# Performance work log

Measured on AMD Instinct MI355X. Metric: run time of the kernel, lower is better.

Reference implementation:

```python
import jax, jax.numpy as jnp
import numpy as np

D_MODEL = 1024
N_HEADS = 16
HEAD_DIM = D_MODEL // N_HEADS
CHUNK = 128
B, T = 2, 2048


def setup_inputs() -> dict:
    key = jax.random.key(0)
    ks = jax.random.split(key, 5)
    x = jax.random.normal(ks[0], (B, T, D_MODEL), dtype=jnp.float32)
    mk = lambda k: jax.random.normal(k, (D_MODEL, D_MODEL), dtype=jnp.float32) * 0.02
    return {"x": x, "Wq": mk(ks[1]), "Wk": mk(ks[2]), "Wv": mk(ks[3]), "Wo": mk(ks[4])}


def _chunked_causal_attention(q, k, v, cs):
    # q,k,v: [B,H,T,D] fp32. Streaming online-softmax over kv chunks (flash-attn style).
    Bq, H, Tq, D = q.shape
    n = Tq // cs  # T divisible by chunk_size
    inv_sqrt_d = 1.0 / (D ** 0.5)
    qc = jnp.moveaxis(q.reshape(Bq, H, n, cs, D), 2, 0)  # [n,B,H,cs,D]
    kc = jnp.moveaxis(k.reshape(Bq, H, n, cs, D), 2, 0)
    vc = jnp.moveaxis(v.reshape(Bq, H, n, cs, D), 2, 0)
    ar = jnp.arange(cs)

    def per_q(qi, qb):  # qb: [B,H,cs,D]
        q_idx = qi * cs + ar

        def step(carry, kv):
            m, l, o = carry
            ki, kb, vb = kv
            s = jnp.einsum('bhqd,bhkd->bhqk', qb, kb) * inv_sqrt_d
            k_idx = ki * cs + ar
            causal = q_idx[:, None] >= k_idx[None, :]
            s = jnp.where(causal, s, -jnp.inf)
            s_max = jnp.max(s, axis=-1, keepdims=True)
            m_new = jnp.maximum(m, s_max)
            # guard fully-masked chunks (m_new = -inf)
            m_safe = jnp.where(jnp.isneginf(m_new), 0.0, m_new)
            alpha = jnp.exp(m - m_safe)
            p = jnp.exp(s - m_safe)
            o = o * alpha + jnp.einsum('bhqk,bhkd->bhqd', p, vb)
            l = l * alpha + jnp.sum(p, axis=-1, keepdims=True)
            return (m_new, l, o), None

        init = (jnp.full((Bq, H, cs, 1), -jnp.inf, dtype=jnp.float32),
                jnp.zeros((Bq, H, cs, 1), dtype=jnp.float32),
                jnp.zeros_like(qb))
        (m, l, o), _ = jax.lax.scan(step, init, (jnp.arange(n), kc, vc))
        return o / jnp.maximum(l, 1e-9)

    out = jax.vmap(per_q)(jnp.arange(n), qc)  # [n,B,H,cs,D]
    return jnp.moveaxis(out, 0, 2).reshape(Bq, H, Tq, D)


def reference(x, Wq, Wk, Wv, Wo):
    Bx, Tx, C = x.shape
    def heads(w):
        return (x @ w.T).reshape(Bx, Tx, N_HEADS, HEAD_DIM).transpose(0, 2, 1, 3)
    q, k, v = heads(Wq), heads(Wk), heads(Wv)
    y = _chunked_causal_attention(q, k, v, CHUNK)  # [B,H,T,D]
    y = y.transpose(0, 2, 1, 3).reshape(Bx, Tx, C)
    return y @ Wo.T
```

## Files before the change

kernel.cpp:

```cpp
#include <hip/hip_runtime.h>
#include <hip/hip_bf16.h>
#include <stdint.h>

typedef __bf16 bf16;
typedef __bf16 bf16x8 __attribute__((ext_vector_type(8)));
typedef __bf16 bf16x4 __attribute__((ext_vector_type(4)));
typedef float  f32x4  __attribute__((ext_vector_type(4)));

#define DM 1024
#define NH 16
#define HD 64
#define TT 2048

#define QSCALE 0.18033688011112042f

__global__ void cvt_all(const float* __restrict__ x,  const float* __restrict__ wq,
                        const float* __restrict__ wk, const float* __restrict__ wv,
                        const float* __restrict__ wo,
                        bf16* __restrict__ xb,  bf16* __restrict__ wqb,
                        bf16* __restrict__ wkb, bf16* __restrict__ wvb,
                        bf16* __restrict__ wob) {
  const int i = (blockIdx.x * blockDim.x + threadIdx.x) * 4;
  const float* src; bf16* dst; int off;
  if (i < 4194304)      { src = x;  dst = xb;  off = i; }
  else {
    const int j = i - 4194304;
    const int w = j >> 20;
    off = j & 1048575;
    src = (w == 0) ? wq : (w == 1) ? wk : (w == 2) ? wv : wo;
    dst = (w == 0) ? wqb : (w == 1) ? wkb : (w == 2) ? wvb : wob;
  }
  const float4 v = *reinterpret_cast<const float4*>(src + off);
  bf16x4 o = { (bf16)v.x, (bf16)v.y, (bf16)v.z, (bf16)v.w };
  *reinterpret_cast<bf16x4*>(dst + off) = o;
}

static __device__ __forceinline__ void gload_lds16(const bf16* g, bf16* l) {
  __builtin_amdgcn_global_load_lds(
      (__attribute__((address_space(1))) void*)g,
      (__attribute__((address_space(3))) void*)l, 16, 0, 0);
}

static __device__ __forceinline__ int swzb(int lin) {
  return lin ^ (((lin >> 7) & 7) << 4);
}

__launch_bounds__(256, 3)
__global__ void gemm_qkv(const bf16* __restrict__ X, const bf16* __restrict__ Wq,
                         const bf16* __restrict__ Wk, const bf16* __restrict__ Wv,
                         bf16* __restrict__ Qb, bf16* __restrict__ Kb,
                         bf16* __restrict__ Vtb) {
  __shared__ bf16 As[128 * 32];
  __shared__ bf16 Bs[128 * 32];
  const int tid  = threadIdx.x;
  const int lane = tid & 63;
  const int wv   = tid >> 6;
  const int lg   = lane >> 4, lc = lane & 15;
  const int m0   = blockIdx.x * 128;
  const int ng   = blockIdx.y * 128;
  const int which = ng >> 10;
  const bf16* W = (which == 0) ? Wq : ((which == 1) ? Wk : Wv);
  const int n0 = ng & 1023;
  const int wm = wv >> 1, wn = wv & 1;

  f32x4 acc[4][4] = {};

  for (int k0 = 0; k0 < DM; k0 += 32) {
#pragma unroll
    for (int c = 0; c < 2; ++c) {
      const int e   = wv * 512 + c * 2048 + lane * 8;
      const int row = e >> 5, col = e & 31;
      gload_lds16(X + (size_t)(m0 + row) * DM + k0 + col, &As[wv * 512 + c * 2048]);
      gload_lds16(W + (size_t)(n0 + row) * DM + k0 + col, &Bs[wv * 512 + c * 2048]);
    }
    __syncthreads();
    bf16x8 a[4], b[4];
#pragma unroll
    for (int i = 0; i < 4; ++i)
      a[i] = *reinterpret_cast<const bf16x8*>(&As[(wm * 64 + i * 16 + lc) * 32 + lg * 8]);
#pragma unroll
    for (int j = 0; j < 4; ++j)
      b[j] = *reinterpret_cast<const bf16x8*>(&Bs[(wn * 64 + j * 16 + lc) * 32 + lg * 8]);
#pragma unroll
    for (int i = 0; i < 4; ++i)
#pragma unroll
      for (int j = 0; j < 4; ++j)
        acc[i][j] = __builtin_amdgcn_mfma_f32_16x16x32_bf16(a[i], b[j], acc[i][j], 0, 0, 0);
    __syncthreads();
  }

#pragma unroll
  for (int i = 0; i < 4; ++i) {
    const int mg = m0 + wm * 64 + i * 16 + lg * 4;
    const int bb = mg >> 11, t = mg & 2047;
#pragma unroll
    for (int j = 0; j < 4; ++j) {
      const int nl = n0 + wn * 64 + j * 16 + lc;
      const int h = nl >> 6, d = nl & 63;
      const int bh = bb * NH + h;
      const f32x4 v = acc[i][j];
      if (which == 0) {
        bf16* p = Qb + ((size_t)bh * TT + t) * HD + d;
#pragma unroll
        for (int r = 0; r < 4; ++r) p[r * HD] = (bf16)(v[r] * QSCALE);
      } else if (which == 1) {
        bf16* p = Kb + ((size_t)bh * TT + t) * HD + d;
#pragma unroll
        for (int r = 0; r < 4; ++r) p[r * HD] = (bf16)v[r];
      } else {
        bf16x4 pk = { (bf16)v[0], (bf16)v[1], (bf16)v[2], (bf16)v[3] };
        *reinterpret_cast<bf16x4*>(Vtb + ((size_t)bh * HD + d) * TT + t) = pk;
      }
    }
  }
}

#define KPAD 72

__launch_bounds__(256, 3)
__global__ void attn_fwd(const bf16* __restrict__ Qb, const bf16* __restrict__ Kb,
                         const bf16* __restrict__ Vtb, bf16* __restrict__ Yb) {
  __shared__ bf16 Ks[2][4096];
  __shared__ bf16 Vs[2][4096];
  __shared__ bf16 Ps[4][16 * KPAD];

  const int tid  = threadIdx.x;
  const int lane = tid & 63;
  const int wv   = tid >> 6;
  const int lg   = lane >> 4;
  const int lc   = lane & 15;
  const int bh   = blockIdx.x & 31;
  const int qblk = 31 - (blockIdx.x >> 5);
  const int q0   = qblk * 64;
  const int NT   = qblk + 1;

  const bf16* Qg = Qb  + (size_t)bh * TT * HD;
  const bf16* Kg = Kb  + (size_t)bh * TT * HD;
  const bf16* Vg = Vtb + (size_t)bh * HD * TT;

  const bf16x8 qf0 = *reinterpret_cast<const bf16x8*>(
      Qg + (size_t)(q0 + wv * 16 + lc) * HD + 0  + lg * 8);
  const bf16x8 qf1 = *reinterpret_cast<const bf16x8*>(
      Qg + (size_t)(q0 + wv * 16 + lc) * HD + 32 + lg * 8);

  int dstb[2], koff[2], voff[2];
#pragma unroll
  for (int c = 0; c < 2; ++c) {
    const int base = (wv * 2 + c) * 1024;
    const int lin  = base + lane * 16;
    dstb[c] = base;
    koff[c] = swzb(lin);
    voff[c] = (lin >> 7) * (TT * 2) + (swzb(lin) & 127);
  }

  auto STAGE = [&](int b, int kv) {
#pragma unroll
    for (int c = 0; c < 2; ++c) {
      gload_lds16((const bf16*)((const char*)Kg + (size_t)kv * 8192 + koff[c]),
                  (bf16*)((char*)Ks[b] + dstb[c]));
      gload_lds16((const bf16*)((const char*)Vg + (size_t)kv * 128 + voff[c]),
                  (bf16*)((char*)Vs[b] + dstb[c]));
    }
  };

  f32x4 o[4] = {};
  float m_run = -INFINITY, l_run = 0.f;
  bf16* Pw = Ps[wv];
  const int b_ = bh >> 4, h_ = bh & 15;
  const int qw = q0 + wv * 16;

  STAGE(0, 0);

  int cur = 0;
  for (int ti = 0; ti < NT; ++ti) {
    const int k0 = ti * 64;

    if (ti + 1 < NT) {
      STAGE(cur ^ 1, ti + 1);
      asm volatile("s_waitcnt vmcnt(4)" ::: "memory");
    } else {
      asm volatile("s_waitcnt vmcnt(0)" ::: "memory");
    }
    __builtin_amdgcn_s_barrier();
    __builtin_amdgcn_sched_barrier(0);

    const char* ksb = (const char*)Ks[cur];
    const char* vsb = (const char*)Vs[cur];

    f32x4 s[4] = {};
    __builtin_amdgcn_s_setprio(1);
#pragma unroll
    for (int kvf = 0; kvf < 4; ++kvf) {
      const bf16x8 k0f = *reinterpret_cast<const bf16x8*>(
          ksb + swzb((kvf * 16 + lc) * 128 + lg * 16));
      s[kvf] = __builtin_amdgcn_mfma_f32_16x16x32_bf16(k0f, qf0, s[kvf], 0, 0, 0);
      const bf16x8 k1f = *reinterpret_cast<const bf16x8*>(
          ksb + swzb((kvf * 16 + lc) * 128 + 64 + lg * 16));
      s[kvf] = __builtin_amdgcn_mfma_f32_16x16x32_bf16(k1f, qf1, s[kvf], 0, 0, 0);
    }
    __builtin_amdgcn_s_setprio(0);

    if (k0 + 63 > qw) {
      const int q = qw + lc;
#pragma unroll
      for (int kvf = 0; kvf < 4; ++kvf)
#pragma unroll
        for (int r = 0; r < 4; ++r)
          if (k0 + kvf * 16 + lg * 4 + r > q) s[kvf][r] = -INFINITY;
    }

    float t0 = fmaxf(fmaxf(s[0][0], s[0][1]), fmaxf(s[0][2], s[0][3]));
    float t1 = fmaxf(fmaxf(s[1][0], s[1][1]), fmaxf(s[1][2], s[1][3]));
    float t2 = fmaxf(fmaxf(s[2][0], s[2][1]), fmaxf(s[2][2], s[2][3]));
    float t3 = fmaxf(fmaxf(s[3][0], s[3][1]), fmaxf(s[3][2], s[3][3]));
    float rmax = fmaxf(fmaxf(t0, t1), fmaxf(t2, t3));
    rmax = fmaxf(rmax, __shfl_xor(rmax, 16));
    rmax = fmaxf(rmax, __shfl_xor(rmax, 32));

    const float mn = fmaxf(m_run, rmax);
    const float alpha = __builtin_amdgcn_exp2f(m_run - mn);
    m_run = mn;

#pragma unroll
    for (int kvf = 0; kvf < 4; ++kvf)
#pragma unroll
      for (int r = 0; r < 4; ++r)
        s[kvf][r] = __builtin_amdgcn_exp2f(s[kvf][r] - mn);

#pragma unroll
    for (int df = 0; df < 4; ++df)
#pragma unroll
      for (int r = 0; r < 4; ++r) o[df][r] *= alpha;

#pragma unroll
    for (int kvf = 0; kvf < 4; ++kvf) {
      bf16x4 pk = { (bf16)s[kvf][0], (bf16)s[kvf][1],
                    (bf16)s[kvf][2], (bf16)s[kvf][3] };
      *reinterpret_cast<bf16x4*>(&Pw[lc * KPAD + kvf * 16 + lg * 4]) = pk;
    }

    __builtin_amdgcn_s_setprio(1);
#pragma unroll
    for (int ks = 0; ks < 2; ++ks) {
      const bf16x8 pf = *reinterpret_cast<const bf16x8*>(
          &Pw[lc * KPAD + ks * 32 + lg * 8]);
#pragma unroll
      for (int df = 0; df < 4; ++df) {
        const bf16x8 vf = *reinterpret_cast<const bf16x8*>(
            vsb + swzb((df * 16 + lc) * 128 + ks * 64 + lg * 16));
        o[df] = __builtin_amdgcn_mfma_f32_16x16x32_bf16(vf, pf, o[df], 0, 0, 0);
      }
    }
    __builtin_amdgcn_s_setprio(0);

    float u0 = (s[0][0] + s[0][1]) + (s[0][2] + s[0][3]);
    float u1 = (s[1][0] + s[1][1]) + (s[1][2] + s[1][3]);
    float u2 = (s[2][0] + s[2][1]) + (s[2][2] + s[2][3]);
    float u3 = (s[3][0] + s[3][1]) + (s[3][2] + s[3][3]);
    float rsum = (u0 + u1) + (u2 + u3);
    rsum += __shfl_xor(rsum, 16);
    rsum += __shfl_xor(rsum, 32);
    l_run = l_run * alpha + rsum;

    __builtin_amdgcn_s_barrier();
    cur ^= 1;
  }

  {
    const float linv = 1.f / fmaxf(l_run, 1e-9f);
    const int q = qw + lc;
#pragma unroll
    for (int df = 0; df < 4; ++df) {
      bf16x4 yv = { (bf16)(o[df][0] * linv), (bf16)(o[df][1] * linv),
                    (bf16)(o[df][2] * linv), (bf16)(o[df][3] * linv) };
      *reinterpret_cast<bf16x4*>(
          Yb + ((size_t)(b_ * TT + q)) * DM + h_ * HD + df * 16 + lg * 4) = yv;
    }
  }
}

__launch_bounds__(256, 2)
__global__ void gemm_out(const bf16* __restrict__ Y, const bf16* __restrict__ Wo,
                         float* __restrict__ Out) {
  __shared__ bf16 As[64 * 32];
  __shared__ bf16 Bs[128 * 32];
  const int tid  = threadIdx.x;
  const int lane = tid & 63;
  const int wv   = tid >> 6;
  const int lg   = lane >> 4, lc = lane & 15;
  const int m0   = blockIdx.x * 64;
  const int n0   = blockIdx.y * 128;
  const int wm = wv >> 1, wn = wv & 1;

  f32x4 acc[2][4] = {};

  for (int k0 = 0; k0 < DM; k0 += 32) {
    {
      const int e   = wv * 512 + lane * 8;
      const int row = e >> 5, col = e & 31;
      gload_lds16(Y + (size_t)(m0 + row) * DM + k0 + col, &As[wv * 512]);
    }
#pragma unroll
    for (int c = 0; c < 2; ++c) {
      const int e   = wv * 1024 + c * 512 + lane * 8;
      const int row = e >> 5, col = e & 31;
      gload_lds16(Wo + (size_t)(n0 + row) * DM + k0 + col, &Bs[wv * 1024 + c * 512]);
    }
    __syncthreads();
    bf16x8 a[2], b[4];
#pragma unroll
    for (int i = 0; i < 2; ++i)
      a[i] = *reinterpret_cast<const bf16x8*>(&As[(wm * 32 + i * 16 + lc) * 32 + lg * 8]);
#pragma unroll
    for (int j = 0; j < 4; ++j)
      b[j] = *reinterpret_cast<const bf16x8*>(&Bs[(wn * 64 + j * 16 + lc) * 32 + lg * 8]);
#pragma unroll
    for (int i = 0; i < 2; ++i)
#pragma unroll
      for (int j = 0; j < 4; ++j)
        acc[i][j] = __builtin_amdgcn_mfma_f32_16x16x32_bf16(a[i], b[j], acc[i][j], 0, 0, 0);
    __syncthreads();
  }

#pragma unroll
  for (int i = 0; i < 2; ++i) {
    const int mg = m0 + wm * 32 + i * 16 + lg * 4;
#pragma unroll
    for (int j = 0; j < 4; ++j) {
      const int n = n0 + wn * 64 + j * 16 + lc;
#pragma unroll
      for (int r = 0; r < 4; ++r)
        Out[(size_t)(mg + r) * DM + n] = acc[i][j][r];
    }
  }
}

extern "C" void kernel_launch(void* const* d_in, const int* in_sizes, int n_in,
                              void* d_out, int out_size, void* d_ws, size_t ws_size,
                              hipStream_t stream) {
  const float* x  = (const float*)d_in[0];
  const float* Wq = (const float*)d_in[1];
  const float* Wk = (const float*)d_in[2];
  const float* Wv = (const float*)d_in[3];
  const float* Wo = (const float*)d_in[4];
  float* out = (float*)d_out;
  char* ws = (char*)d_ws;
  const size_t MB = 1024 * 1024;

  bf16* xb  = (bf16*)(ws + 0);
  bf16* wqb = (bf16*)(ws + 8  * MB);
  bf16* wkb = (bf16*)(ws + 10 * MB);
  bf16* wvb = (bf16*)(ws + 12 * MB);
  bf16* wob = (bf16*)(ws + 14 * MB);
  bf16* Qb  = (bf16*)(ws + 16 * MB);
  bf16* Kb  = (bf16*)(ws + 24 * MB);
  bf16* Vtb = (bf16*)(ws + 32 * MB);
  bf16* yb  = xb;

  cvt_all<<<8192, 256, 0, stream>>>(x, Wq, Wk, Wv, Wo, xb, wqb, wkb, wvb, wob);
  gemm_qkv<<<dim3(32, 24), 256, 0, stream>>>(xb, wqb, wkb, wvb, Qb, Kb, Vtb);
  attn_fwd<<<1024, 256, 0, stream>>>(Qb, Kb, Vtb, yb);
  gemm_out<<<dim3(64, 8), 256, 0, stream>>>(yb, wob, out);
}
```

Measured before the change: 107.7 us.

## Rewrite attention with 32x32 MFMA, register P exchange, lazy rescale, persistent scheduler

```diff
diff --git a/kernel.cpp b/kernel.cpp
--- a/kernel.cpp
+++ b/kernel.cpp
@@ -6,6 +6,8 @@
 typedef __bf16 bf16x8 __attribute__((ext_vector_type(8)));
 typedef __bf16 bf16x4 __attribute__((ext_vector_type(4)));
 typedef float  f32x4  __attribute__((ext_vector_type(4)));
+typedef float  f32x16 __attribute__((ext_vector_type(16)));
+typedef unsigned int u32;
 
 #define DM 1024
 #define NH 16
@@ -43,6 +45,15 @@
 
 static __device__ __forceinline__ int swzb(int lin) {
   return lin ^ (((lin >> 7) & 7) << 4);
+}
+
+static __device__ __forceinline__ u32 cvtpk(float lo, float hi) {
+  u32 r;
+  asm("v_cvt_pk_bf16_f32 %0, %1, %2" : "=v"(r) : "v"(lo), "v"(hi));
+  return r;
+}
+static __device__ __forceinline__ void plswap(u32& a, u32& b) {
+  asm("v_permlane32_swap_b32 %0, %1" : "+v"(a), "+v"(b));
 }
 
 __launch_bounds__(256, 3)
@@ -115,166 +126,208 @@
   }
 }
 
-#define KPAD 72
-
-__launch_bounds__(256, 3)
+#define NCHUNK 1024
+#define MF32(a, b, c) __builtin_amdgcn_mfma_f32_32x32x16_bf16((a), (b), (c), 0, 0, 0)
+
+__launch_bounds__(128, 2)
 __global__ void attn_fwd(const bf16* __restrict__ Qb, const bf16* __restrict__ Kb,
-                         const bf16* __restrict__ Vtb, bf16* __restrict__ Yb) {
+                         const bf16* __restrict__ Vtb, bf16* __restrict__ Yb,
+                         u32* __restrict__ ctr) {
   __shared__ bf16 Ks[2][4096];
   __shared__ bf16 Vs[2][4096];
-  __shared__ bf16 Ps[4][16 * KPAD];
+  __shared__ int sIdx;
 
   const int tid  = threadIdx.x;
   const int lane = tid & 63;
   const int wv   = tid >> 6;
-  const int lg   = lane >> 4;
-  const int lc   = lane & 15;
-  const int bh   = blockIdx.x & 31;
-  const int qblk = 31 - (blockIdx.x >> 5);
-  const int q0   = qblk * 64;
-  const int NT   = qblk + 1;
-
-  const bf16* Qg = Qb  + (size_t)bh * TT * HD;
-  const bf16* Kg = Kb  + (size_t)bh * TT * HD;
-  const bf16* Vg = Vtb + (size_t)bh * HD * TT;
-
-  const bf16x8 qf0 = *reinterpret_cast<const bf16x8*>(
-      Qg + (size_t)(q0 + wv * 16 + lc) * HD + 0  + lg * 8);
-  const bf16x8 qf1 = *reinterpret_cast<const bf16x8*>(
-      Qg + (size_t)(q0 + wv * 16 + lc) * HD + 32 + lg * 8);
-
-  int dstb[2], koff[2], voff[2];
-#pragma unroll
-  for (int c = 0; c < 2; ++c) {
-    const int base = (wv * 2 + c) * 1024;
+  const int m31  = lane & 31;
+  const int hi   = lane >> 5;
+  const int hi16 = hi << 4;
+  const int hi4  = hi << 2;
+  const int xr   = (m31 & 7) << 4;
+  const int kRow = m31 * 128;
+  int colx[4];
+#pragma unroll
+  for (int i = 0; i < 4; ++i) colx[i] = (i * 32 + hi16) ^ xr;
+
+  int dstb[4], koff[4], voff[4];
+#pragma unroll
+  for (int c = 0; c < 4; ++c) {
+    const int base = (wv * 4 + c) * 1024;
     const int lin  = base + lane * 16;
     dstb[c] = base;
     koff[c] = swzb(lin);
     voff[c] = (lin >> 7) * (TT * 2) + (swzb(lin) & 127);
   }
 
-  auto STAGE = [&](int b, int kv) {
-#pragma unroll
-    for (int c = 0; c < 2; ++c) {
-      gload_lds16((const bf16*)((const char*)Kg + (size_t)kv * 8192 + koff[c]),
-                  (bf16*)((char*)Ks[b] + dstb[c]));
-      gload_lds16((const bf16*)((const char*)Vg + (size_t)kv * 128 + voff[c]),
-                  (bf16*)((char*)Vs[b] + dstb[c]));
-    }
-  };
-
-  f32x4 o[4] = {};
-  float m_run = -INFINITY, l_run = 0.f;
-  bf16* Pw = Ps[wv];
-  const int b_ = bh >> 4, h_ = bh & 15;
-  const int qw = q0 + wv * 16;
-
-  STAGE(0, 0);
-
-  int cur = 0;
-  for (int ti = 0; ti < NT; ++ti) {
-    const int k0 = ti * 64;
-
-    if (ti + 1 < NT) {
-      STAGE(cur ^ 1, ti + 1);
-      asm volatile("s_waitcnt vmcnt(4)" ::: "memory");
-    } else {
-      asm volatile("s_waitcnt vmcnt(0)" ::: "memory");
-    }
-    __builtin_amdgcn_s_barrier();
-    __builtin_amdgcn_sched_barrier(0);
-
-    const char* ksb = (const char*)Ks[cur];
-    const char* vsb = (const char*)Vs[cur];
-
-    f32x4 s[4] = {};
-    __builtin_amdgcn_s_setprio(1);
-#pragma unroll
-    for (int kvf = 0; kvf < 4; ++kvf) {
-      const bf16x8 k0f = *reinterpret_cast<const bf16x8*>(
-          ksb + swzb((kvf * 16 + lc) * 128 + lg * 16));
-      s[kvf] = __builtin_amdgcn_mfma_f32_16x16x32_bf16(k0f, qf0, s[kvf], 0, 0, 0);
-      const bf16x8 k1f = *reinterpret_cast<const bf16x8*>(
-          ksb + swzb((kvf * 16 + lc) * 128 + 64 + lg * 16));
-      s[kvf] = __builtin_amdgcn_mfma_f32_16x16x32_bf16(k1f, qf1, s[kvf], 0, 0, 0);
-    }
-    __builtin_amdgcn_s_setprio(0);
-
-    if (k0 + 63 > qw) {
-      const int q = qw + lc;
-#pragma unroll
-      for (int kvf = 0; kvf < 4; ++kvf)
-#pragma unroll
-        for (int r = 0; r < 4; ++r)
-          if (k0 + kvf * 16 + lg * 4 + r > q) s[kvf][r] = -INFINITY;
-    }
-
-    float t0 = fmaxf(fmaxf(s[0][0], s[0][1]), fmaxf(s[0][2], s[0][3]));
-    float t1 = fmaxf(fmaxf(s[1][0], s[1][1]), fmaxf(s[1][2], s[1][3]));
-    float t2 = fmaxf(fmaxf(s[2][0], s[2][1]), fmaxf(s[2][2], s[2][3]));
-    float t3 = fmaxf(fmaxf(s[3][0], s[3][1]), fmaxf(s[3][2], s[3][3]));
-    float rmax = fmaxf(fmaxf(t0, t1), fmaxf(t2, t3));
-    rmax = fmaxf(rmax, __shfl_xor(rmax, 16));
-    rmax = fmaxf(rmax, __shfl_xor(rmax, 32));
-
-    const float mn = fmaxf(m_run, rmax);
-    const float alpha = __builtin_amdgcn_exp2f(m_run - mn);
-    m_run = mn;
-
-#pragma unroll
-    for (int kvf = 0; kvf < 4; ++kvf)
-#pragma unroll
-      for (int r = 0; r < 4; ++r)
-        s[kvf][r] = __builtin_amdgcn_exp2f(s[kvf][r] - mn);
-
-#pragma unroll
-    for (int df = 0; df < 4; ++df)
-#pragma unroll
-      for (int r = 0; r < 4; ++r) o[df][r] *= alpha;
-
-#pragma unroll
-    for (int kvf = 0; kvf < 4; ++kvf) {
-      bf16x4 pk = { (bf16)s[kvf][0], (bf16)s[kvf][1],
-                    (bf16)s[kvf][2], (bf16)s[kvf][3] };
-      *reinterpret_cast<bf16x4*>(&Pw[lc * KPAD + kvf * 16 + lg * 4]) = pk;
-    }
-
-    __builtin_amdgcn_s_setprio(1);
-#pragma unroll
-    for (int ks = 0; ks < 2; ++ks) {
-      const bf16x8 pf = *reinterpret_cast<const bf16x8*>(
-          &Pw[lc * KPAD + ks * 32 + lg * 8]);
-#pragma unroll
-      for (int df = 0; df < 4; ++df) {
-        const bf16x8 vf = *reinterpret_cast<const bf16x8*>(
-            vsb + swzb((df * 16 + lc) * 128 + ks * 64 + lg * 16));
-        o[df] = __builtin_amdgcn_mfma_f32_16x16x32_bf16(vf, pf, o[df], 0, 0, 0);
+  for (;;) {
+    if (tid == 0) sIdx = (int)atomicAdd(ctr, 1u);
+    __syncthreads();
+    const int idx = sIdx;
+    if (idx >= NCHUNK) break;
+
+    const int qc  = 31 - (idx >> 5);
+    const int bh  = idx & 31;
+    const int NT  = qc + 1;
+    const int qb0 = qc * 64 + wv * 32;
+    const int qrow = qb0 + m31;
+
+    const bf16* Qg = Qb  + (size_t)bh * TT * HD;
+    const bf16* Kg = Kb  + (size_t)bh * TT * HD;
+    const bf16* Vg = Vtb + (size_t)bh * HD * TT;
+
+    bf16x8 qr0 = *reinterpret_cast<const bf16x8*>(Qg + (size_t)qrow * HD + 0  + hi * 8);
+    bf16x8 qr1 = *reinterpret_cast<const bf16x8*>(Qg + (size_t)qrow * HD + 16 + hi * 8);
+    bf16x8 qr2 = *reinterpret_cast<const bf16x8*>(Qg + (size_t)qrow * HD + 32 + hi * 8);
+    bf16x8 qr3 = *reinterpret_cast<const bf16x8*>(Qg + (size_t)qrow * HD + 48 + hi * 8);
+
+    f32x16 o0 = {}, o1 = {};
+    float m_run = -INFINITY, l_run = 0.f;
+
+#define STAGE(buf, kv)                                                          \
+    {                                                                           \
+      _Pragma("unroll")                                                         \
+      for (int c = 0; c < 4; ++c) {                                             \
+        gload_lds16((const bf16*)((const char*)Kg + (size_t)(kv) * 8192 + koff[c]), \
+                    (bf16*)((char*)Ks[buf] + dstb[c]));                         \
+        gload_lds16((const bf16*)((const char*)Vg + (size_t)(kv) * 128 + voff[c]),  \
+                    (bf16*)((char*)Vs[buf] + dstb[c]));                         \
+      }                                                                         \
+    }
+
+    STAGE(0, 0);
+    int cur = 0;
+    for (int ti = 0; ti < NT; ++ti) {
+      if (ti + 1 < NT) {
+        STAGE(cur ^ 1, ti + 1);
+        asm volatile("s_waitcnt vmcnt(8)" ::: "memory");
+      } else {
+        asm volatile("s_waitcnt vmcnt(0)" ::: "memory");
       }
-    }
-    __builtin_amdgcn_s_setprio(0);
-
-    float u0 = (s[0][0] + s[0][1]) + (s[0][2] + s[0][3]);
-    float u1 = (s[1][0] + s[1][1]) + (s[1][2] + s[1][3]);
-    float u2 = (s[2][0] + s[2][1]) + (s[2][2] + s[2][3]);
-    float u3 = (s[3][0] + s[3][1]) + (s[3][2] + s[3][3]);
-    float rsum = (u0 + u1) + (u2 + u3);
-    rsum += __shfl_xor(rsum, 16);
-    rsum += __shfl_xor(rsum, 32);
-    l_run = l_run * alpha + rsum;
-
-    __builtin_amdgcn_s_barrier();
-    cur ^= 1;
-  }
-
-  {
-    const float linv = 1.f / fmaxf(l_run, 1e-9f);
-    const int q = qw + lc;
-#pragma unroll
-    for (int df = 0; df < 4; ++df) {
-      bf16x4 yv = { (bf16)(o[df][0] * linv), (bf16)(o[df][1] * linv),
-                    (bf16)(o[df][2] * linv), (bf16)(o[df][3] * linv) };
-      *reinterpret_cast<bf16x4*>(
-          Yb + ((size_t)(b_ * TT + q)) * DM + h_ * HD + df * 16 + lg * 4) = yv;
+      __builtin_amdgcn_s_barrier();
+      __builtin_amdgcn_sched_barrier(0);
+
+      const char* ksb = (const char*)Ks[cur];
+      const char* vsb = (const char*)Vs[cur];
+      const int k0 = ti * 64;
+      const bool live = (k0 <= qb0 + 31);
+
+      if (live) {
+        f32x16 s0 = {}, s1 = {};
+        __builtin_amdgcn_s_setprio(1);
+        {
+          bf16x8 kf;
+          kf = *reinterpret_cast<const bf16x8*>(ksb + kRow + colx[0]); s0 = MF32(kf, qr0, s0);
+          kf = *reinterpret_cast<const bf16x8*>(ksb + kRow + colx[1]); s0 = MF32(kf, qr1, s0);
+          kf = *reinterpret_cast<const bf16x8*>(ksb + kRow + colx[2]); s0 = MF32(kf, qr2, s0);
+          kf = *reinterpret_cast<const bf16x8*>(ksb + kRow + colx[3]); s0 = MF32(kf, qr3, s0);
+          kf = *reinterpret_cast<const bf16x8*>(ksb + 4096 + kRow + colx[0]); s1 = MF32(kf, qr0, s1);
+          kf = *reinterpret_cast<const bf16x8*>(ksb + 4096 + kRow + colx[1]); s1 = MF32(kf, qr1, s1);
+          kf = *reinterpret_cast<const bf16x8*>(ksb + 4096 + kRow + colx[2]); s1 = MF32(kf, qr2, s1);
+          kf = *reinterpret_cast<const bf16x8*>(ksb + 4096 + kRow + colx[3]); s1 = MF32(kf, qr3, s1);
+        }
+        __builtin_amdgcn_s_setprio(0);
+
+        if (k0 + 63 > qb0) {
+#pragma unroll
+          for (int r = 0; r < 16; ++r) {
+            const int kvl = (r & 3) + 8 * (r >> 2) + hi4;
+            if (k0 + kvl > qrow)      s0[r] = -INFINITY;
+            if (k0 + 32 + kvl > qrow) s1[r] = -INFINITY;
+          }
+        }
+
+        float q0m = fmaxf(fmaxf(s0[0], s0[1]),  fmaxf(s0[2], s0[3]));
+        float q1m = fmaxf(fmaxf(s0[4], s0[5]),  fmaxf(s0[6], s0[7]));
+        float q2m = fmaxf(fmaxf(s0[8], s0[9]),  fmaxf(s0[10], s0[11]));
+        float q3m = fmaxf(fmaxf(s0[12], s0[13]), fmaxf(s0[14], s0[15]));
+        float q4m = fmaxf(fmaxf(s1[0], s1[1]),  fmaxf(s1[2], s1[3]));
+        float q5m = fmaxf(fmaxf(s1[4], s1[5]),  fmaxf(s1[6], s1[7]));
+        float q6m = fmaxf(fmaxf(s1[8], s1[9]),  fmaxf(s1[10], s1[11]));
+        float q7m = fmaxf(fmaxf(s1[12], s1[13]), fmaxf(s1[14], s1[15]));
+        float pm = fmaxf(fmaxf(fmaxf(q0m, q1m), fmaxf(q2m, q3m)),
+                         fmaxf(fmaxf(q4m, q5m), fmaxf(q6m, q7m)));
+        pm = fmaxf(pm, __shfl_xor(pm, 32));
+
+        const int need = pm > m_run + 8.f;
+        if (__any(need)) {
+          const float mn = fmaxf(m_run, pm);
+          const float al = __builtin_amdgcn_exp2f(m_run - mn);
+          m_run = mn; l_run *= al;
+#pragma unroll
+          for (int r = 0; r < 16; ++r) { o0[r] *= al; o1[r] *= al; }
+        }
+
+#pragma unroll
+        for (int r = 0; r < 16; ++r) {
+          s0[r] = __builtin_amdgcn_exp2f(s0[r] - m_run);
+          s1[r] = __builtin_amdgcn_exp2f(s1[r] - m_run);
+        }
+
+        union PU { u32 w[4]; bf16x8 v; } pu0, pu1, pu2, pu3;
+        {
+          u32 a0 = cvtpk(s0[0],  s0[1]),  a1 = cvtpk(s0[2],  s0[3]);
+          u32 b0 = cvtpk(s0[4],  s0[5]),  b1 = cvtpk(s0[6],  s0[7]);
+          plswap(a0, b0); plswap(a1, b1);
+          pu0.w[0] = a0; pu0.w[1] = a1; pu0.w[2] = b0; pu0.w[3] = b1;
+          u32 c0 = cvtpk(s0[8],  s0[9]),  c1 = cvtpk(s0[10], s0[11]);
+          u32 d0 = cvtpk(s0[12], s0[13]), d1 = cvtpk(s0[14], s0[15]);
+          plswap(c0, d0); plswap(c1, d1);
+          pu1.w[0] = c0; pu1.w[1] = c1; pu1.w[2] = d0; pu1.w[3] = d1;
+          u32 e0 = cvtpk(s1[0],  s1[1]),  e1 = cvtpk(s1[2],  s1[3]);
+          u32 f0 = cvtpk(s1[4],  s1[5]),  f1 = cvtpk(s1[6],  s1[7]);
+          plswap(e0, f0); plswap(e1, f1);
+          pu2.w[0] = e0; pu2.w[1] = e1; pu2.w[2] = f0; pu2.w[3] = f1;
+          u32 g0 = cvtpk(s1[8],  s1[9]),  g1 = cvtpk(s1[10], s1[11]);
+          u32 h0 = cvtpk(s1[12], s1[13]), h1 = cvtpk(s1[14], s1[15]);
+          plswap(g0, h0); plswap(g1, h1);
+          pu3.w[0] = g0; pu3.w[1] = g1; pu3.w[2] = h0; pu3.w[3] = h1;
+        }
+
+        __builtin_amdgcn_s_setprio(1);
+        {
+          bf16x8 vf;
+          vf = *reinterpret_cast<const bf16x8*>(vsb + kRow + colx[0]);        o0 = MF32(vf, pu0.v, o0);
+          vf = *reinterpret_cast<const bf16x8*>(vsb + 4096 + kRow + colx[0]); o1 = MF32(vf, pu0.v, o1);
+          vf = *reinterpret_cast<const bf16x8*>(vsb + kRow + colx[1]);        o0 = MF32(vf, pu1.v, o0);
+          vf = *reinterpret_cast<const bf16x8*>(vsb + 4096 + kRow + colx[1]); o1 = MF32(vf, pu1.v, o1);
+          vf = *reinterpret_cast<const bf16x8*>(vsb + kRow + colx[2]);        o0 = MF32(vf, pu2.v, o0);
+          vf = *reinterpret_cast<const bf16x8*>(vsb + 4096 + kRow + colx[2]); o1 = MF32(vf, pu2.v, o1);
+          vf = *reinterpret_cast<const bf16x8*>(vsb + kRow + colx[3]);        o0 = MF32(vf, pu3.v, o0);
+          vf = *reinterpret_cast<const bf16x8*>(vsb + 4096 + kRow + colx[3]); o1 = MF32(vf, pu3.v, o1);
+        }
+        __builtin_amdgcn_s_setprio(0);
+
+        float u0 = (s0[0] + s0[1]) + (s0[2] + s0[3]);
+        float u1 = (s0[4] + s0[5]) + (s0[6] + s0[7]);
+        float u2 = (s0[8] + s0[9]) + (s0[10] + s0[11]);
+        float u3 = (s0[12] + s0[13]) + (s0[14] + s0[15]);
+        float u4 = (s1[0] + s1[1]) + (s1[2] + s1[3]);
+        float u5 = (s1[4] + s1[5]) + (s1[6] + s1[7]);
+        float u6 = (s1[8] + s1[9]) + (s1[10] + s1[11]);
+        float u7 = (s1[12] + s1[13]) + (s1[14] + s1[15]);
+        float rsum = ((u0 + u1) + (u2 + u3)) + ((u4 + u5) + (u6 + u7));
+        rsum += __shfl_xor(rsum, 32);
+        l_run += rsum;
+      }
+
+      __builtin_amdgcn_s_barrier();
+      cur ^= 1;
+    }
+#undef STAGE
+
+    {
+      const float linv = 1.f / fmaxf(l_run, 1e-9f);
+      bf16* yrow = Yb + ((size_t)((bh >> 4) * TT + qrow)) * DM + (bh & 15) * HD;
+#pragma unroll
+      for (int rq = 0; rq < 4; ++rq) {
+        bf16x4 y0 = { (bf16)(o0[rq * 4 + 0] * linv), (bf16)(o0[rq * 4 + 1] * linv),
+                      (bf16)(o0[rq * 4 + 2] * linv), (bf16)(o0[rq * 4 + 3] * linv) };
+        *reinterpret_cast<bf16x4*>(yrow + rq * 8 + hi4) = y0;
+        bf16x4 y1 = { (bf16)(o1[rq * 4 + 0] * linv), (bf16)(o1[rq * 4 + 1] * linv),
+                      (bf16)(o1[rq * 4 + 2] * linv), (bf16)(o1[rq * 4 + 3] * linv) };
+        *reinterpret_cast<bf16x4*>(yrow + 32 + rq * 8 + hi4) = y1;
+      }
     }
   }
 }
@@ -355,10 +408,12 @@
   bf16* Qb  = (bf16*)(ws + 16 * MB);
   bf16* Kb  = (bf16*)(ws + 24 * MB);
   bf16* Vtb = (bf16*)(ws + 32 * MB);
+  u32*  ctr = (u32*)(ws + 40 * MB);
   bf16* yb  = xb;
 
+  hipMemsetAsync(ctr, 0, 4, stream);
   cvt_all<<<8192, 256, 0, stream>>>(x, Wq, Wk, Wv, Wo, xb, wqb, wkb, wvb, wob);
   gemm_qkv<<<dim3(32, 24), 256, 0, stream>>>(xb, wqb, wkb, wvb, Qb, Kb, Vtb);
-  attn_fwd<<<1024, 256, 0, stream>>>(Qb, Kb, Vtb, yb);
+  attn_fwd<<<1024, 128, 0, stream>>>(Qb, Kb, Vtb, yb, ctr);
   gemm_out<<<dim3(64, 8), 256, 0, stream>>>(yb, wob, out);
 }
```

Result: slower. 130.5 us (+21.2%).
